# Performance work log

Measured on AMD Instinct MI355X. Metric: run time of the kernel, lower is better.

Reference implementation:

```python
import jax, jax.numpy as jnp
import numpy as np

K = 7            # involution kernel size
GC = 16          # group_channels (canonical involution)
EPS = 1e-6


def ln_cf(x, w, b):
    # channels_first LayerNorm over channel dim (axis=1), as in ConvNeXt utils
    u = jnp.mean(x, axis=1, keepdims=True)
    s = jnp.mean((x - u) ** 2, axis=1, keepdims=True)
    xn = (x - u) / jnp.sqrt(s + EPS)
    return w[:, None, None] * xn + b[:, None, None]


def gelu(x):
    return jax.nn.gelu(x, approximate=False)  # torch nn.GELU default (erf)


def involution(x, w1, b1, w2, b2):
    # x: (B,C,H,W). Kernel-generating head: 1x1 conv -> ReLU -> 1x1 conv.
    B, C, H, W = x.shape
    G = C // GC
    mid = jnp.einsum('bchw,mc->bmhw', x, w1) + b1[None, :, None, None]
    mid = jax.nn.relu(mid)
    wk = jnp.einsum('bmhw,km->bkhw', mid, w2) + b2[None, :, None, None]
    wk = wk.reshape(B, G, K * K, H, W)  # per-pixel, per-group K*K kernels
    pad = (K - 1) // 2
    xp = jnp.pad(x, ((0, 0), (0, 0), (pad, pad), (pad, pad)))
    out = jnp.zeros((B, G, GC, H, W), dtype=x.dtype)
    # accumulate over the K*K spatial offsets (fixed small loop, no big unfold)
    for idx in range(K * K):
        i, j = divmod(idx, K)
        xs = xp[:, :, i:i + H, j:j + W].reshape(B, G, GC, H, W)
        out = out + wk[:, :, idx][:, :, None] * xs
    return out.reshape(B, C, H, W)


def setup_inputs() -> dict:
    key = jax.random.key(0)
    ks = jax.random.split(key, 8)
    B, C, O, H, Wd = 4, 128, 256, 128, 128
    mid = C // 4
    G = C // GC
    sc = 0.05
    return {
        'x': jax.random.normal(ks[0], (B, C, H, Wd), jnp.float32),
        'w1': jax.random.normal(ks[1], (mid, C), jnp.float32) * sc,
        'b1': jnp.zeros((mid,), jnp.float32),
        'w2': jax.random.normal(ks[2], (K * K * G, mid), jnp.float32) * sc,
        'b2': jnp.zeros((K * K * G,), jnp.float32),
        'ln1_w': jnp.ones((C,), jnp.float32),
        'ln1_b': jnp.zeros((C,), jnp.float32),
        'conv_w': jax.random.normal(ks[3], (O, C), jnp.float32) * sc,
        'ln2_w': jnp.ones((O,), jnp.float32),
        'ln2_b': jnp.zeros((O,), jnp.float32),
        'map_w': jax.random.normal(ks[4], (O, C), jnp.float32) * sc,
        'map_b': jnp.zeros((O,), jnp.float32),
        'ln3_w': jnp.ones((O,), jnp.float32),
        'ln3_b': jnp.zeros((O,), jnp.float32),
    }


def reference(x, w1, b1, w2, b2, ln1_w, ln1_b, conv_w, ln2_w, ln2_b,
              map_w, map_b, ln3_w, ln3_b):
    # invblock: Involution -> LayerNorm(channels_first) -> GELU
    x1 = involution(x, w1, b1, w2, b2)
    x1 = gelu(ln_cf(x1, ln1_w, ln1_b))
    # conv_block: 1x1 conv (no bias) -> LayerNorm
    x1 = ln_cf(jnp.einsum('bchw,oc->bohw', x1, conv_w), ln2_w, ln2_b)
    # mapping (channels differ): 1x1 conv (bias) -> LayerNorm
    xm = jnp.einsum('bchw,oc->bohw', x, map_w) + map_b[None, :, None, None]
    xm = ln_cf(xm, ln3_w, ln3_b)
    return gelu(x1 + xm)
```

## Files before the change

### kernel.cpp

```cpp
#include <hip/hip_runtime.h>

typedef unsigned short ushort_t;
typedef unsigned int uint_t;

#define NB 4
#define NC 128
#define NH 128
#define NW 128
#define NPIX 65536
#define NMID 32
#define NKK 49
#define NK 392
#define NKP 400
#define NO 256
#define LN_EPS 1e-6f

typedef __attribute__((ext_vector_type(8))) short short8;
typedef __attribute__((ext_vector_type(4))) float floatx4;

__device__ __forceinline__ float bf2f(ushort_t u) {
    union { uint_t i; float f; } v; v.i = ((uint_t)u) << 16; return v.f;
}
__device__ __forceinline__ float bf2f_lo(uint_t u) {
    union { uint_t i; float f; } v; v.i = u << 16; return v.f;
}
__device__ __forceinline__ float bf2f_hi(uint_t u) {
    union { uint_t i; float f; } v; v.i = u & 0xffff0000u; return v.f;
}
__device__ __forceinline__ ushort_t f2bf(float f) {
    union { float f; uint_t i; } v; v.f = f;
    uint_t x = v.i;
    uint_t r = (x + 0x7FFFu + ((x >> 16) & 1u)) >> 16;
    return (ushort_t)r;
}
__device__ __forceinline__ float gelu_f(float x) {
    return 0.5f * x * (1.0f + erff(x * 0.70710678118654752f));
}
__device__ __forceinline__ float ldin(const void* p, int i, int isf32) {
    return isf32 ? ((const float*)p)[i] : bf2f(((const ushort_t*)p)[i]);
}

__global__ void kdetect(const uint_t* __restrict__ xw, int* __restrict__ flag) {
    int lane = threadIdx.x;
    int cnt = 0;
    for (int j = 0; j < 8; j++) {
        uint_t w = xw[lane * 8 + j];
        uint_t e = (w >> 7) & 0xffu;
        if (e >= 110u && e <= 135u) cnt++;
    }
    for (int d = 1; d < 64; d <<= 1) cnt += __shfl_xor(cnt, d);
    if (lane == 0) flag[0] = (cnt < 256) ? 1 : 0;
}

__global__ void ksentinel(uint_t* __restrict__ out, int nwords) {
    int i = blockIdx.x * 256 + threadIdx.x;
    if (i < nwords) out[i] = 0x40004000u;
}

__global__ __launch_bounds__(256) void ktrans(const void* __restrict__ x,
                                              ushort_t* __restrict__ xT,
                                              const int* __restrict__ flag) {
    int isf32 = flag[0];
    int b = blockIdx.z, h = blockIdx.y;
    int wchunk = blockIdx.x & 1, cchunk = blockIdx.x >> 1;
    int w0 = wchunk << 6, c0 = cchunk << 5;
    __shared__ ushort_t tile[32][66];
    int tx = threadIdx.x & 63, ty = threadIdx.x >> 6;
    for (int r = 0; r < 32; r += 4) {
        int idx = (((b * NC + c0 + r + ty) * NH) + h) * NW + w0 + tx;
        tile[r + ty][tx] = isf32 ? f2bf(((const float*)x)[idx])
                                 : ((const ushort_t*)x)[idx];
    }
    __syncthreads();
    int cc = threadIdx.x & 31, wq = threadIdx.x >> 5;
    for (int pp = 0; pp < 64; pp += 8) {
        int wx = pp + wq;
        xT[((size_t)((b * NH + h) * NW) + w0 + wx) * NC + c0 + cc] = tile[cc][wx];
    }
}

__global__ __launch_bounds__(256) void kprep(const void* w1, const void* w2,
                                             const void* b1, const void* b2,
                                             const void* ln1w, const void* ln1b,
                                             const void* ln2w, const void* ln2b,
                                             const void* map_b,
                                             const void* ln3w, const void* ln3b,
                                             const int* __restrict__ flag,
                                             ushort_t* __restrict__ w1b,
                                             ushort_t* __restrict__ w2b,
                                             float* __restrict__ b1f,
                                             float* __restrict__ b2f,
                                             float* __restrict__ ln1wf,
                                             float* __restrict__ ln1bf,
                                             float* __restrict__ ln2wf,
                                             float* __restrict__ ln2bf,
                                             float* __restrict__ mbf,
                                             float* __restrict__ ln3wf,
                                             float* __restrict__ ln3bf) {
    int isf32 = flag[0];
    int i = blockIdx.x * 256 + threadIdx.x;
    if (i < NMID * NC) w1b[i] = f2bf(ldin(w1, i, isf32));
    if (i < NKP * NMID) w2b[i] = (i < NK * NMID) ? f2bf(ldin(w2, i, isf32))
                                                 : (ushort_t)0;
    if (i < NMID) b1f[i] = ldin(b1, i, isf32);
    if (i < NKP)  b2f[i] = (i < NK) ? ldin(b2, i, isf32) : 0.f;
    if (i < NC) { ln1wf[i] = ldin(ln1w, i, isf32); ln1bf[i] = ldin(ln1b, i, isf32); }
    if (i < NO) {
        ln2wf[i] = ldin(ln2w, i, isf32); ln2bf[i] = ldin(ln2b, i, isf32);
        mbf[i]   = ldin(map_b, i, isf32);
        ln3wf[i] = ldin(ln3w, i, isf32); ln3bf[i] = ldin(ln3b, i, isf32);
    }
}

__global__ __launch_bounds__(256) void kfrag(const void* conv_w, const void* map_w,
                                             const int* __restrict__ flag,
                                             ushort_t* __restrict__ wfrag) {
    int isf32 = flag[0];
    int cid = blockIdx.x * 256 + threadIdx.x;
    int lane = cid & 63, nt = (cid >> 6) & 3, br = (cid >> 8) & 1;
    int kb = (cid >> 9) & 3, w = (cid >> 11) & 3;
    int o = w * 64 + nt * 16 + (lane & 15);
    int ch0 = kb * 32 + (lane >> 4) * 8;
    const void* src = br ? map_w : conv_w;
    ushort_t* dst = wfrag + (size_t)cid * 8;
#pragma unroll
    for (int j = 0; j < 8; j++)
        dst[j] = f2bf(ldin(src, o * NC + ch0 + j, isf32));
}

__global__ __launch_bounds__(256) void k1a(const ushort_t* __restrict__ xT,
                                           const ushort_t* __restrict__ w1b,
                                           const float* __restrict__ b1f,
                                           const ushort_t* __restrict__ w2b,
                                           const float* __restrict__ b2f,
                                           ushort_t* __restrict__ wkT) {
    __shared__ ushort_t midbuf[64 * 32];
    __shared__ ushort_t wkstage[NKP * 66];

    int t = threadIdx.x;
    int lane = t & 63;
    int w = __builtin_amdgcn_readfirstlane(t >> 6);
    int l16 = lane & 15, quad = lane >> 4;
    int tileid = blockIdx.x;
    int tilex = tileid & 15, tiley = (tileid >> 4) & 15, b = tileid >> 8;
    int h0 = tiley * 8, w0 = tilex * 8;

    int lpx_a = 16 * w + l16;
    int py = lpx_a >> 3, pxx = lpx_a & 7;
    const ushort_t* abase = xT + (size_t)((b * NH + h0 + py) * NW + w0 + pxx) * NC + quad * 8;
    floatx4 am0 = (floatx4)0.f, am1 = (floatx4)0.f;
#pragma unroll
    for (int kb = 0; kb < 4; kb++) {
        short8 a   = *(const short8*)(abase + kb * 32);
        short8 b0  = *(const short8*)(w1b + (l16) * NC + kb * 32 + quad * 8);
        short8 b1v = *(const short8*)(w1b + (16 + l16) * NC + kb * 32 + quad * 8);
        am0 = __builtin_amdgcn_mfma_f32_16x16x32_bf16(a, b0, am0, 0, 0, 0);
        am1 = __builtin_amdgcn_mfma_f32_16x16x32_bf16(a, b1v, am1, 0, 0, 0);
    }
    {
        float bia0 = b1f[l16], bia1 = b1f[16 + l16];
#pragma unroll
        for (int r = 0; r < 4; r++) {
            int m = 16 * w + quad * 4 + r;
            midbuf[m * 32 + l16]      = f2bf(fmaxf(am0[r] + bia0, 0.f));
            midbuf[m * 32 + 16 + l16] = f2bf(fmaxf(am1[r] + bia1, 0.f));
        }
    }
    __syncthreads();

    short8 aM = *(const short8*)(midbuf + (16 * w + l16) * 32 + quad * 8);
#pragma unroll
    for (int nt = 0; nt < 25; nt++) {
        int n = nt * 16 + l16;
        short8 bw = *(const short8*)(w2b + n * 32 + quad * 8);
        floatx4 c = __builtin_amdgcn_mfma_f32_16x16x32_bf16(aM, bw, (floatx4)0.f, 0, 0, 0);
        float bias = b2f[n];
#pragma unroll
        for (int r = 0; r < 4; r++)
            wkstage[n * 66 + 16 * w + quad * 4 + r] = f2bf(c[r] + bias);
    }
    __syncthreads();

    int krow = t >> 5, px2 = t & 31;
    for (int it = 0; it < 50; it++) {
        int k = it * 8 + krow;
        uint_t v = *(const uint_t*)&wkstage[k * 66 + 2 * px2];
        *(uint_t*)&wkT[(size_t)k * NPIX + tileid * 64 + 2 * px2] = v;
    }
}

__global__ __launch_bounds__(512) void k1b(const ushort_t* __restrict__ xT,
                                           const ushort_t* __restrict__ wkT,
                                           const float* __restrict__ ln1wf,
                                           const float* __restrict__ ln1bf,
                                           ushort_t* __restrict__ y1) {
    __shared__ __align__(16) char smem[50432];
    uint4* x8   = (uint4*)smem;
    float* sred = (float*)smem;

    int t = threadIdx.x;
    int lane = t & 63;
    int w = __builtin_amdgcn_readfirstlane(t >> 6);
    int tileid = blockIdx.x;
    int tilex = tileid & 15, tiley = (tileid >> 4) & 15, b = tileid >> 8;
    int h0 = tiley * 8, w0 = tilex * 8;
    int py = lane >> 3, pxx = lane & 7;

    const ushort_t* wkbase = wkT + (size_t)(w * NKK) * NPIX + tileid * 64 + lane;
    uint_t wkp[25];
#pragma unroll
    for (int j = 0; j < 24; j++) {
        uint_t lo = wkbase[(size_t)(2 * j) * NPIX];
        uint_t hi = wkbase[(size_t)(2 * j + 1) * NPIX];
        wkp[j] = lo | (hi << 16);
    }
    wkp[24] = wkbase[(size_t)48 * NPIX];

    for (int it = 0; it < 7; it++) {
        int idx = it * 512 + t;
        if (idx < 3136) {
            int oct = idx & 15, hp = idx >> 4;
            int hy = hp / 14, hx = hp - hy * 14;
            int gh = h0 + hy - 3, gw = w0 + hx - 3;
            uint4 v = make_uint4(0u, 0u, 0u, 0u);
            if ((unsigned)gh < (unsigned)NH && (unsigned)gw < (unsigned)NW) {
                v = *(const uint4*)&xT[(size_t)((b * NH + gh) * NW + gw) * NC + 8 * oct];
            }
            x8[oct * 197 + hp] = v;
        }
    }
    __syncthreads();

    int base0 = py * 14 + pxx;
    float a[16];
#pragma unroll
    for (int j = 0; j < 16; j++) a[j] = 0.f;

#pragma unroll
    for (int tap = 0; tap < NKK; tap++) {
        float wkf = (tap & 1) ? bf2f((ushort_t)(wkp[tap >> 1] >> 16))
                              : bf2f((ushort_t)(wkp[tap >> 1] & 0xffffu));
        int xa = base0 + (tap / 7) * 14 + (tap % 7);
        uint4 u0 = x8[(2 * w) * 197 + xa];
        uint4 u1 = x8[(2 * w + 1) * 197 + xa];
        a[0]  = fmaf(wkf, bf2f_lo(u0.x), a[0]);
        a[1]  = fmaf(wkf, bf2f_hi(u0.x), a[1]);
        a[2]  = fmaf(wkf, bf2f_lo(u0.y), a[2]);
        a[3]  = fmaf(wkf, bf2f_hi(u0.y), a[3]);
        a[4]  = fmaf(wkf, bf2f_lo(u0.z), a[4]);
        a[5]  = fmaf(wkf, bf2f_hi(u0.z), a[5]);
        a[6]  = fmaf(wkf, bf2f_lo(u0.w), a[6]);
        a[7]  = fmaf(wkf, bf2f_hi(u0.w), a[7]);
        a[8]  = fmaf(wkf, bf2f_lo(u1.x), a[8]);
        a[9]  = fmaf(wkf, bf2f_hi(u1.x), a[9]);
        a[10] = fmaf(wkf, bf2f_lo(u1.y), a[10]);
        a[11] = fmaf(wkf, bf2f_hi(u1.y), a[11]);
        a[12] = fmaf(wkf, bf2f_lo(u1.z), a[12]);
        a[13] = fmaf(wkf, bf2f_hi(u1.z), a[13]);
        a[14] = fmaf(wkf, bf2f_lo(u1.w), a[14]);
        a[15] = fmaf(wkf, bf2f_hi(u1.w), a[15]);
    }
    __syncthreads();

    float s = 0.f, sq = 0.f;
#pragma unroll
    for (int j = 0; j < 16; j++) { s += a[j]; sq += a[j] * a[j]; }
    sred[(w * 64 + lane) * 2]     = s;
    sred[(w * 64 + lane) * 2 + 1] = sq;
    __syncthreads();
    float ts = 0.f, tq = 0.f;
#pragma unroll
    for (int r = 0; r < 8; r++) {
        ts += sred[(r * 64 + lane) * 2];
        tq += sred[(r * 64 + lane) * 2 + 1];
    }
    float mean = ts * (1.0f / NC);
    float var = tq * (1.0f / NC) - mean * mean;
    float rstd = rsqrtf(var + LN_EPS);

    int p = (b * NH + h0 + py) * NW + w0 + pxx;
    uint_t pk[8];
#pragma unroll
    for (int j = 0; j < 8; j++) {
        int c0 = 16 * w + 2 * j;
        float g0 = gelu_f((a[2 * j] - mean) * rstd * ln1wf[c0] + ln1bf[c0]);
        float g1 = gelu_f((a[2 * j + 1] - mean) * rstd * ln1wf[c0 + 1] + ln1bf[c0 + 1]);
        pk[j] = (uint_t)f2bf(g0) | ((uint_t)f2bf(g1) << 16);
    }
    uint4* dst = (uint4*)(y1 + (size_t)p * NC + 16 * w);
    dst[0] = make_uint4(pk[0], pk[1], pk[2], pk[3]);
    dst[1] = make_uint4(pk[4], pk[5], pk[6], pk[7]);
}

__global__ __launch_bounds__(64) void k1_fused(const ushort_t* __restrict__ xT,
                                               const ushort_t* __restrict__ w1b,
                                               const float* __restrict__ b1f,
                                               const ushort_t* __restrict__ w2b,
                                               const float* __restrict__ b2f,
                                               const float* __restrict__ ln1wf,
                                               const float* __restrict__ ln1bf,
                                               ushort_t* __restrict__ y1) {
    __shared__ ushort_t midbuf[16 * 32];
    __shared__ ushort_t wkbuf[16 * NKP];

    int lane = threadIdx.x;
    int l16 = lane & 15, quad = lane >> 4;
    int b = blockIdx.z;
    int h0 = blockIdx.y * 2, w0 = blockIdx.x * 8;

    int Pa = (b * NH + h0 + (l16 >> 3)) * NW + w0 + (l16 & 7);
    const ushort_t* abase = xT + (size_t)Pa * NC + quad * 8;
    floatx4 am0 = (floatx4)0.f, am1 = (floatx4)0.f;
#pragma unroll
    for (int kb = 0; kb < 4; kb++) {
        short8 a   = *(const short8*)(abase + kb * 32);
        short8 b0  = *(const short8*)(w1b + (l16) * NC + kb * 32 + quad * 8);
        short8 b1v = *(const short8*)(w1b + (16 + l16) * NC + kb * 32 + quad * 8);
        am0 = __builtin_amdgcn_mfma_f32_16x16x32_bf16(a, b0, am0, 0, 0, 0);
        am1 = __builtin_amdgcn_mfma_f32_16x16x32_bf16(a, b1v, am1, 0, 0, 0);
    }
    {
        float bia0 = b1f[l16], bia1 = b1f[16 + l16];
#pragma unroll
        for (int r = 0; r < 4; r++) {
            int m = quad * 4 + r;
            midbuf[m * 32 + l16]      = f2bf(fmaxf(am0[r] + bia0, 0.f));
            midbuf[m * 32 + 16 + l16] = f2bf(fmaxf(am1[r] + bia1, 0.f));
        }
    }
    __syncthreads();

    short8 aM = *(const short8*)(midbuf + l16 * 32 + quad * 8);
#pragma unroll
    for (int nt = 0; nt < 25; nt++) {
        int n = nt * 16 + l16;
        short8 bw = *(const short8*)(w2b + n * 32 + quad * 8);
        floatx4 c = __builtin_amdgcn_mfma_f32_16x16x32_bf16(aM, bw, (floatx4)0.f, 0, 0, 0);
        float bias = b2f[n];
#pragma unroll
        for (int r = 0; r < 4; r++)
            wkbuf[(quad * 4 + r) * NKP + n] = f2bf(c[r] + bias);
    }
    __syncthreads();

    int g = lane >> 3;
    float l1w0 = ln1wf[2 * lane], l1w1 = ln1wf[2 * lane + 1];
    float l1b0 = ln1bf[2 * lane], l1b1 = ln1bf[2 * lane + 1];

    for (int i = 0; i < 16; i++) {
        int hh0 = h0 + (i >> 3), ww0 = w0 + (i & 7);
        int p = (b * NH + hh0) * NW + ww0;
        const ushort_t* wkrow = wkbuf + i * NKP + g * NKK;
        float a0 = 0.f, a1 = 0.f;
#pragma unroll
        for (int dy = -3; dy <= 3; dy++) {
            int hh = hh0 + dy;
            if ((unsigned)hh >= (unsigned)NH) continue;
#pragma unroll
            for (int dx = -3; dx <= 3; dx++) {
                int ww = ww0 + dx;
                if ((unsigned)ww >= (unsigned)NW) continue;
                float wkv = bf2f(wkrow[(dy + 3) * 7 + (dx + 3)]);
                uint_t xp = *(const uint_t*)(xT + ((size_t)(p + dy * NW + dx)) * NC + 2 * lane);
                a0 = fmaf(wkv, bf2f((ushort_t)(xp & 0xffffu)), a0);
                a1 = fmaf(wkv, bf2f((ushort_t)(xp >> 16)), a1);
            }
        }
        float s = a0 + a1, sq = a0 * a0 + a1 * a1;
#pragma unroll
        for (int d = 1; d < 64; d <<= 1) {
            s  += __shfl_xor(s, d);
            sq += __shfl_xor(sq, d);
        }
        float mean = s * (1.0f / NC);
        float var = sq * (1.0f / NC) - mean * mean;
        float rstd = rsqrtf(var + LN_EPS);
        float g0 = gelu_f((a0 - mean) * rstd * l1w0 + l1b0);
        float g1 = gelu_f((a1 - mean) * rstd * l1w1 + l1b1);
        uint_t pk = (uint_t)f2bf(g0) | ((uint_t)f2bf(g1) << 16);
        *(uint_t*)(y1 + (size_t)p * NC + 2 * lane) = pk;
    }
}

__global__ __launch_bounds__(256, 2) void k23(const ushort_t* __restrict__ y1,
                                              const ushort_t* __restrict__ xT,
                                              const ushort_t* __restrict__ wfrag,
                                              const float* __restrict__ mbf,
                                              const float* __restrict__ ln2wf,
                                              const float* __restrict__ ln2bf,
                                              const float* __restrict__ ln3wf,
                                              const float* __restrict__ ln3bf,
                                              void* __restrict__ out,
                                              const int* __restrict__ flag) {
    __shared__ __align__(16) float tbuf[4 * 2 * 320];

    int isf32 = flag[0];
    int t = threadIdx.x;
    int lane = t & 63;
    int w = __builtin_amdgcn_readfirstlane(t >> 6);
    int quad = lane >> 4, l16 = lane & 15;

    int P0 = blockIdx.x * 64;
    int pw = P0 + w * 16;
    const ushort_t* aYp = y1 + (size_t)(pw + l16) * NC + quad * 8;
    const ushort_t* aXp = xT + (size_t)(pw + l16) * NC + quad * 8;
    const ushort_t* bb  = wfrag + (size_t)lane * 8;

    floatx4 accC[16], accM[16];
#pragma unroll
    for (int n4 = 0; n4 < 16; n4++) { accC[n4] = (floatx4)0.f; accM[n4] = (floatx4)0.f; }

#pragma unroll
    for (int kb = 0; kb < 4; kb++) {
        short8 aY = *(const short8*)(aYp + kb * 32);
        short8 aX = *(const short8*)(aXp + kb * 32);
#pragma unroll
        for (int n4 = 0; n4 < 16; n4++) {
            const ushort_t* bp = bb + (size_t)(((n4 >> 2) * 2048 + kb * 512 + (n4 & 3) * 64)) * 8;
            short8 bc = *(const short8*)bp;
            short8 bm = *(const short8*)(bp + 256 * 8);
            accC[n4] = __builtin_amdgcn_mfma_f32_16x16x32_bf16(aY, bc, accC[n4], 0, 0, 0);
            accM[n4] = __builtin_amdgcn_mfma_f32_16x16x32_bf16(aX, bm, accM[n4], 0, 0, 0);
        }
    }

#pragma unroll
    for (int n4 = 0; n4 < 16; n4++) {
        float mb = mbf[n4 * 16 + l16];
#pragma unroll
        for (int r = 0; r < 4; r++) accM[n4][r] += mb;
    }

    floatx4 s1 = (floatx4)0.f, q1 = (floatx4)0.f, s2 = (floatx4)0.f, q2 = (floatx4)0.f;
#pragma unroll
    for (int n4 = 0; n4 < 16; n4++)
#pragma unroll
        for (int r = 0; r < 4; r++) {
            float a = accC[n4][r], m = accM[n4][r];
            s1[r] += a; q1[r] += a * a;
            s2[r] += m; q2[r] += m * m;
        }
#pragma unroll
    for (int d = 1; d < 16; d <<= 1) {
#pragma unroll
        for (int r = 0; r < 4; r++) {
            s1[r] += __shfl_xor(s1[r], d);
            q1[r] += __shfl_xor(q1[r], d);
            s2[r] += __shfl_xor(s2[r], d);
            q2[r] += __shfl_xor(q2[r], d);
        }
    }
    floatx4 m1, r1, m2, r2;
#pragma unroll
    for (int r = 0; r < 4; r++) {
        m1[r] = s1[r] * (1.0f / NO);
        r1[r] = rsqrtf(q1[r] * (1.0f / NO) - m1[r] * m1[r] + LN_EPS);
        m2[r] = s2[r] * (1.0f / NO);
        r2[r] = rsqrtf(q2[r] * (1.0f / NO) - m2[r] * m2[r] + LN_EPS);
    }

    int batch = pw >> 14;
    int plocal = pw & 16383;
    int o_l = lane >> 2, px4 = (lane & 3) * 4;
    float* tb0 = tbuf + w * 640;

#pragma unroll
    for (int n4 = 0; n4 < 16; n4++) {
        int o = n4 * 16 + l16;
        float l2w = ln2wf[o], l2b = ln2bf[o];
        float l3w = ln3wf[o], l3b = ln3bf[o];
        float* tb = tb0 + (n4 & 1) * 320;
        float4 gv;
        {
            float v1, v2;
            v1 = (accC[n4][0] - m1[0]) * r1[0] * l2w + l2b;
            v2 = (accM[n4][0] - m2[0]) * r2[0] * l3w + l3b;
            gv.x = gelu_f(v1 + v2);
            v1 = (accC[n4][1] - m1[1]) * r1[1] * l2w + l2b;
            v2 = (accM[n4][1] - m2[1]) * r2[1] * l3w + l3b;
            gv.y = gelu_f(v1 + v2);
            v1 = (accC[n4][2] - m1[2]) * r1[2] * l2w + l2b;
            v2 = (accM[n4][2] - m2[2]) * r2[2] * l3w + l3b;
            gv.z = gelu_f(v1 + v2);
            v1 = (accC[n4][3] - m1[3]) * r1[3] * l2w + l2b;
            v2 = (accM[n4][3] - m2[3]) * r2[3] * l3w + l3b;
            gv.w = gelu_f(v1 + v2);
        }
        *(float4*)(tb + l16 * 20 + quad * 4) = gv;
        asm volatile("s_waitcnt lgkmcnt(0)" ::: "memory");
        float4 tv = *(const float4*)(tb + o_l * 20 + px4);
        asm volatile("" ::: "memory");
        size_t oi = ((size_t)(batch * NO + n4 * 16 + o_l) << 14) + plocal + px4;
        if (isf32) {
            *(float4*)((float*)out + oi) = tv;
        } else {
            uint_t p0 = (uint_t)f2bf(tv.x) | ((uint_t)f2bf(tv.y) << 16);
            uint_t p1 = (uint_t)f2bf(tv.z) | ((uint_t)f2bf(tv.w) << 16);
            *(uint2*)((ushort_t*)out + oi) = make_uint2(p0, p1);
        }
    }
}

extern "C" void kernel_launch(void* const* d_in, const int* in_sizes, int n_in,
                              void* d_out, int out_size, void* d_ws, size_t ws_size,
                              hipStream_t stream) {
    const void* x      = d_in[0];
    const void* w1     = d_in[1];
    const void* b1     = d_in[2];
    const void* w2     = d_in[3];
    const void* b2     = d_in[4];
    const void* ln1w   = d_in[5];
    const void* ln1b   = d_in[6];
    const void* conv_w = d_in[7];
    const void* ln2w   = d_in[8];
    const void* ln2b   = d_in[9];
    const void* map_w  = d_in[10];
    const void* map_b  = d_in[11];
    const void* ln3w   = d_in[12];
    const void* ln3b   = d_in[13];

    char* ws = (char*)d_ws;
    ushort_t* xT    = (ushort_t*)(ws);
    ushort_t* y1    = (ushort_t*)(ws + 16777216);
    ushort_t* wfrag = (ushort_t*)(ws + 33554432);
    ushort_t* w1b   = (ushort_t*)(ws + 33685504);
    ushort_t* w2b   = (ushort_t*)(ws + 33693696);
    float*    b1f   = (float*)(ws + 33719296);
    float*    b2f   = (float*)(ws + 33719424);
    float*    ln1wf = (float*)(ws + 33721024);
    float*    ln1bf = (float*)(ws + 33721536);
    float*    mbf   = (float*)(ws + 33722048);
    float*    ln2wf = (float*)(ws + 33723072);
    float*    ln2bf = (float*)(ws + 33724096);
    float*    ln3wf = (float*)(ws + 33725120);
    float*    ln3bf = (float*)(ws + 33726144);
    int*      flag  = (int*)(ws + 33727168);
    const size_t NEED_SMALL = 33727184;
    ushort_t* wkT   = (ushort_t*)(ws + 33727232);
    const size_t NEED_BIG = 33727232 + (size_t)NKP * NPIX * 2;

    if (ws_size < NEED_SMALL) {
        int nwords = out_size / 2;
        ksentinel<<<(nwords + 255) / 256, 256, 0, stream>>>((uint_t*)d_out, nwords);
        return;
    }

    kdetect<<<1, 64, 0, stream>>>((const uint_t*)x, flag);
    kprep<<<128, 256, 0, stream>>>(w1, w2, b1, b2, ln1w, ln1b,
                                   ln2w, ln2b, map_b, ln3w, ln3b, flag,
                                   w1b, w2b, b1f, b2f, ln1wf, ln1bf,
                                   ln2wf, ln2bf, mbf, ln3wf, ln3bf);
    kfrag<<<32, 256, 0, stream>>>(conv_w, map_w, flag, wfrag);
    ktrans<<<dim3(8, 128, 4), 256, 0, stream>>>(x, xT, flag);

    if (ws_size >= NEED_BIG) {
        k1a<<<1024, 256, 0, stream>>>(xT, w1b, b1f, w2b, b2f, wkT);
        k1b<<<1024, 512, 0, stream>>>(xT, wkT, ln1wf, ln1bf, y1);
    } else {
        k1_fused<<<dim3(16, 64, 4), 64, 0, stream>>>(xT, w1b, b1f, w2b, b2f,
                                                     ln1wf, ln1bf, y1);
    }

    k23<<<NPIX / 64, 256, 0, stream>>>(y1, xT, wfrag, mbf,
                                       ln2wf, ln2bf, ln3wf, ln3bf, d_out, flag);
}
```

Before: 234.2 us.

## Stage k23 weight fragments in LDS with double-buffered async loads

Reorders the precomputed weight fragments so each k-block is contiguous. k23 now cooperatively copies each block into a 64KB double-buffered LDS area with global_load_lds, instead of every wave re-reading the fragments from global memory. The activation A-fragments are prefetched into registers up front, and the LDS transpose in the epilogue is removed so stores go out directly from the MFMA layout. The 64KB of LDS per block likely limits occupancy, and the direct stores are less coalesced (16-byte chunks per output channel row).

```diff
diff --git a/kernel.cpp b/kernel.cpp
--- a/kernel.cpp
+++ b/kernel.cpp
@@ -38,6 +38,11 @@
 }
 __device__ __forceinline__ float ldin(const void* p, int i, int isf32) {
     return isf32 ? ((const float*)p)[i] : bf2f(((const ushort_t*)p)[i]);
+}
+__device__ __forceinline__ void gload_lds16(const void* g, void* l) {
+    __builtin_amdgcn_global_load_lds(
+        (const __attribute__((address_space(1))) void*)g,
+        (__attribute__((address_space(3))) void*)l, 16, 0, 0);
 }
 
 __global__ void kdetect(const uint_t* __restrict__ xw, int* __restrict__ flag) {
@@ -117,9 +122,8 @@
                                              ushort_t* __restrict__ wfrag) {
     int isf32 = flag[0];
     int cid = blockIdx.x * 256 + threadIdx.x;
-    int lane = cid & 63, nt = (cid >> 6) & 3, br = (cid >> 8) & 1;
-    int kb = (cid >> 9) & 3, w = (cid >> 11) & 3;
-    int o = w * 64 + nt * 16 + (lane & 15);
+    int lane = cid & 63, n4 = (cid >> 6) & 15, br = (cid >> 10) & 1, kb = cid >> 11;
+    int o = n4 * 16 + (lane & 15);
     int ch0 = kb * 32 + (lane >> 4) * 8;
     const void* src = br ? map_w : conv_w;
     ushort_t* dst = wfrag + (size_t)cid * 8;
@@ -392,7 +396,7 @@
                                               const float* __restrict__ ln3bf,
                                               void* __restrict__ out,
                                               const int* __restrict__ flag) {
-    __shared__ __align__(16) float tbuf[4 * 2 * 320];
+    __shared__ __align__(16) char sbuf[65536];
 
     int isf32 = flag[0];
     int t = threadIdx.x;
@@ -404,7 +408,21 @@
     int pw = P0 + w * 16;
     const ushort_t* aYp = y1 + (size_t)(pw + l16) * NC + quad * 8;
     const ushort_t* aXp = xT + (size_t)(pw + l16) * NC + quad * 8;
-    const ushort_t* bb  = wfrag + (size_t)lane * 8;
+
+    {
+        const ushort_t* gsrc = wfrag + (size_t)(w * 512 + lane) * 8;
+        char* ldst = sbuf + (size_t)(w * 512) * 16;
+#pragma unroll
+        for (int i = 0; i < 8; i++)
+            gload_lds16(gsrc + i * 64 * 8, ldst + i * 64 * 16);
+    }
+    short8 aYr[4], aXr[4];
+#pragma unroll
+    for (int kb = 0; kb < 4; kb++) {
+        aYr[kb] = *(const short8*)(aYp + kb * 32);
+        aXr[kb] = *(const short8*)(aXp + kb * 32);
+    }
+    __syncthreads();
 
     floatx4 accC[16], accM[16];
 #pragma unroll
@@ -412,16 +430,24 @@
 
 #pragma unroll
     for (int kb = 0; kb < 4; kb++) {
-        short8 aY = *(const short8*)(aYp + kb * 32);
-        short8 aX = *(const short8*)(aXp + kb * 32);
+        const char* bufr = sbuf + (kb & 1) * 32768;
+        if (kb < 3) {
+            char* bufw = sbuf + ((kb + 1) & 1) * 32768;
+            const ushort_t* gsrc = wfrag + ((size_t)(kb + 1) * 2048 + w * 512 + lane) * 8;
+            char* ldst = bufw + (size_t)(w * 512) * 16;
+#pragma unroll
+            for (int i = 0; i < 8; i++)
+                gload_lds16(gsrc + i * 64 * 8, ldst + i * 64 * 16);
+        }
+        short8 aY = aYr[kb], aX = aXr[kb];
 #pragma unroll
         for (int n4 = 0; n4 < 16; n4++) {
-            const ushort_t* bp = bb + (size_t)(((n4 >> 2) * 2048 + kb * 512 + (n4 & 3) * 64)) * 8;
-            short8 bc = *(const short8*)bp;
-            short8 bm = *(const short8*)(bp + 256 * 8);
+            short8 bc = *(const short8*)(bufr + (size_t)(n4 * 64 + lane) * 16);
+            short8 bm = *(const short8*)(bufr + (size_t)(1024 + n4 * 64 + lane) * 16);
             accC[n4] = __builtin_amdgcn_mfma_f32_16x16x32_bf16(aY, bc, accC[n4], 0, 0, 0);
             accM[n4] = __builtin_amdgcn_mfma_f32_16x16x32_bf16(aX, bm, accM[n4], 0, 0, 0);
         }
+        if (kb < 3) __syncthreads();
     }
 
 #pragma unroll
@@ -460,16 +486,12 @@
     }
 
     int batch = pw >> 14;
-    int plocal = pw & 16383;
-    int o_l = lane >> 2, px4 = (lane & 3) * 4;
-    float* tb0 = tbuf + w * 640;
-
+    int plocal = (pw & 16383) + quad * 4;
 #pragma unroll
     for (int n4 = 0; n4 < 16; n4++) {
         int o = n4 * 16 + l16;
         float l2w = ln2wf[o], l2b = ln2bf[o];
         float l3w = ln3wf[o], l3b = ln3bf[o];
-        float* tb = tb0 + (n4 & 1) * 320;
         float4 gv;
         {
             float v1, v2;
@@ -486,16 +508,12 @@
             v2 = (accM[n4][3] - m2[3]) * r2[3] * l3w + l3b;
             gv.w = gelu_f(v1 + v2);
         }
-        *(float4*)(tb + l16 * 20 + quad * 4) = gv;
-        asm volatile("s_waitcnt lgkmcnt(0)" ::: "memory");
-        float4 tv = *(const float4*)(tb + o_l * 20 + px4);
-        asm volatile("" ::: "memory");
-        size_t oi = ((size_t)(batch * NO + n4 * 16 + o_l) << 14) + plocal + px4;
+        size_t oi = ((size_t)(batch * NO + o) << 14) + plocal;
         if (isf32) {
-            *(float4*)((float*)out + oi) = tv;
+            *(float4*)((float*)out + oi) = gv;
         } else {
-            uint_t p0 = (uint_t)f2bf(tv.x) | ((uint_t)f2bf(tv.y) << 16);
-            uint_t p1 = (uint_t)f2bf(tv.z) | ((uint_t)f2bf(tv.w) << 16);
+            uint_t p0 = (uint_t)f2bf(gv.x) | ((uint_t)f2bf(gv.y) << 16);
+            uint_t p1 = (uint_t)f2bf(gv.z) | ((uint_t)f2bf(gv.w) << 16);
             *(uint2*)((ushort_t*)out + oi) = make_uint2(p0, p1);
         }
     }
```

After: 229.9 us. No clear change (-1.8%).
